# Optimization experiments

Hardware: AMD Instinct MI355X
Metric: run time of the kernel (lower is better)

The kernel has to match this reference:

```python
import jax, jax.numpy as jnp
import numpy as np

CAPACITY_FACTOR = 1.25
TOP_K = 2


def setup_inputs() -> dict:
    key = jax.random.key(0)
    ks = jax.random.split(key, 4)
    B, T, D, H, N = 8, 8192, 512, 512, 32
    x = jax.random.normal(ks[0], (B, T, D), jnp.float32)
    Wg = jax.random.normal(ks[1], (D, N), jnp.float32) * 0.02   # gate (no bias)
    W1 = jax.random.normal(ks[2], (N, D, H), jnp.float32) * 0.02  # stacked expert fc1
    b1 = jnp.zeros((N, H), jnp.float32)
    W2 = jax.random.normal(ks[3], (N, H, D), jnp.float32) * 0.02  # stacked expert fc2
    b2 = jnp.zeros((N, D), jnp.float32)
    return {"x": x, "Wg": Wg, "W1": W1, "b1": b1, "W2": W2, "b2": b2}


def _moe(x, Wg, W1, b1, W2, b2):
    B, T, D = x.shape
    N = Wg.shape[1]
    K = TOP_K
    BT = B * T
    BTK = BT * K
    C = int(np.ceil(CAPACITY_FACTOR * BTK / N))  # capacity per expert (static)

    x_flat = x.reshape(BT, D)
    probs = jax.nn.softmax(x_flat @ Wg, axis=-1)            # [BT, N]
    vals, idx = jax.lax.top_k(probs, K)                     # [BT, K]
    vals = vals / jnp.clip(vals.sum(-1, keepdims=True), 1e-9)  # normalize_gates

    # Assignments in the exact order of the original double loop: pos-major, j-minor.
    a = idx.reshape(BTK)                                    # expert id per assignment
    oh = jax.nn.one_hot(a, N, dtype=jnp.int32)              # [BTK, N]
    rank = jnp.cumsum(oh, axis=0) - oh                      # prior count for each expert
    pos = jnp.take_along_axis(rank, a[:, None], axis=1)[:, 0]  # slot within expert
    keep = pos < C                                          # capacity-limited dispatch
    dest = jnp.where(keep, a * C + pos, N * C)              # OOB sentinel -> dropped
    token = jnp.arange(BTK) // K                            # source token per assignment

    # Dispatch: scatter kept tokens into per-expert capacity buffers [N, C, D].
    buf = jnp.zeros((N * C, D), x.dtype).at[dest].set(x_flat[token], mode="drop")
    buf = buf.reshape(N, C, D)

    # Expert FFN (grouped GEMMs). FeedForwardExpert assumed Linear-ReLU-Linear.
    h = jax.nn.relu(jnp.einsum("ncd,ndh->nch", buf, W1) + b1[:, None, :])
    o = (jnp.einsum("nch,nhd->ncd", h, W2) + b2[:, None, :]).reshape(N * C, D)

    # Combine: gather expert outputs, weight by gates, scatter-add back by token.
    gathered = o[jnp.minimum(dest, N * C - 1)]              # dropped rows zeroed via w
    w = vals.reshape(BTK) * keep.astype(x.dtype)
    y_flat = jax.ops.segment_sum(gathered * w[:, None], token, num_segments=BT)
    contrib = jax.ops.segment_sum(w, token, num_segments=BT)
    # Tokens with no surviving assignment pass through unchanged.
    y_flat = jnp.where(contrib[:, None] <= 1e-12, x_flat, y_flat)
    return y_flat.reshape(B, T, D)


def reference(x, Wg, W1, b1, W2, b2):
    return _moe(x, Wg, W1, b1, W2, b2)
```

## Files before the change

### kernel.cpp

```cpp
#include <hip/hip_runtime.h>
#include <hip/hip_bf16.h>

#define BT 65536
#define DD 512
#define HH 512
#define NE 32
#define CAP 5120
#define BM 64
#define NRB 80

typedef float  f32x4  __attribute__((ext_vector_type(4)));
typedef short  bf16x8 __attribute__((ext_vector_type(8)));

__device__ __forceinline__ unsigned short f2bf(float f){
    unsigned int u = __builtin_bit_cast(unsigned int, f);
    unsigned int r = (u + 0x7fffu + ((u >> 16) & 1u)) >> 16;
    return (unsigned short)r;
}
__device__ __forceinline__ float bf2f(unsigned short h){
    unsigned int u = ((unsigned int)h) << 16;
    return __builtin_bit_cast(float, u);
}

__global__ __launch_bounds__(256) void k_wgprep(
    const float* __restrict__ Wg,
    unsigned short* __restrict__ WgHf, unsigned short* __restrict__ WgLf)
{
    int t = threadIdx.x;
    #pragma unroll
    for (int i = 0; i < 8; i++){
        int entry = i*256 + t;
        int ln = entry & 63;
        unsigned short h[8], l[8];
        #pragma unroll
        for (int j = 0; j < 8; j++){
            int d = ((entry >> 6) & 15)*32 + (ln >> 4)*8 + j;
            int e = (entry >> 10)*16 + (ln & 15);
            float v = Wg[d*NE + e];
            unsigned short hi = f2bf(v);
            h[j] = hi;
            l[j] = f2bf(v - bf2f(hi));
        }
        *(bf16x8*)(WgHf + (size_t)entry*8) = *(bf16x8*)h;
        *(bf16x8*)(WgLf + (size_t)entry*8) = *(bf16x8*)l;
    }
}

__global__ __launch_bounds__(256) void k_prep(
    const float* __restrict__ x, const float* __restrict__ Wg,
    const float* __restrict__ W1, const float* __restrict__ W2,
    const unsigned short* __restrict__ WgHf, const unsigned short* __restrict__ WgLf,
    unsigned short* __restrict__ W1f, unsigned short* __restrict__ W2f,
    int* __restrict__ counts, int* __restrict__ gsl, float* __restrict__ wts,
    unsigned char* __restrict__ flags, unsigned short* __restrict__ xb16)
{
    __shared__ unsigned char XH[32 * 1024];
    __shared__ unsigned char XL[32 * 1024];
    __shared__ float lg2[32 * 33];
    __shared__ int lcnt[NE], lbase[NE];

    int tid = threadIdx.x;

    if (blockIdx.x >= 2048){
        int b = blockIdx.x - 2048;
        int w = b >> 8;
        int e = (b >> 3) & 31;
        int kq = b & 7;
        const float* src = (w ? W2 : W1) + ((size_t)e << 18);
        unsigned short* dst = (w ? W2f : W1f) + ((size_t)e << 18);
        int n4 = (tid & 127) * 4;
        int kh = tid >> 7;
        #pragma unroll 1
        for (int kg = 0; kg < 4; kg++){
            int k0 = kq*64 + (kg*2 + kh)*8;
            float4 rows[8];
            #pragma unroll
            for (int j = 0; j < 8; j++)
                rows[j] = *(const float4*)&src[(size_t)(k0 + j)*512 + n4];
            unsigned short v0[8], v1[8], v2[8], v3[8];
            #pragma unroll
            for (int j = 0; j < 8; j++){
                v0[j] = f2bf(rows[j].x); v1[j] = f2bf(rows[j].y);
                v2[j] = f2bf(rows[j].z); v3[j] = f2bf(rows[j].w);
            }
            int kc = k0 >> 5, lb = ((k0 >> 3) & 3)*16;
            #pragma unroll
            for (int m = 0; m < 4; m++){
                int n = n4 + m;
                int nt = n >> 4, ln = lb + (n & 15);
                const unsigned short* vv = (m==0)?v0:(m==1)?v1:(m==2)?v2:v3;
                *(bf16x8*)(dst + (((size_t)(nt*16 + kc)*64 + ln) << 3)) = *(const bf16x8*)vv;
            }
        }
        return;
    }

    int t0 = blockIdx.x * 32;

    {
        int row = tid >> 3, seg = tid & 7;
        int tok = t0 + row;
        const float* sx = x + (size_t)tok*DD + seg*64;
        char* rbH = (char*)XH + row*1024;
        char* rbL = (char*)XL + row*1024;
        int rsw = (row & 7) << 4;
        #pragma unroll
        for (int jj = 0; jj < 8; jj++){
            float4 a = *(const float4*)(sx + jj*8);
            float4 b = *(const float4*)(sx + jj*8 + 4);
            unsigned short h[8], l[8];
            h[0]=f2bf(a.x); h[1]=f2bf(a.y); h[2]=f2bf(a.z); h[3]=f2bf(a.w);
            h[4]=f2bf(b.x); h[5]=f2bf(b.y); h[6]=f2bf(b.z); h[7]=f2bf(b.w);
            l[0]=f2bf(a.x-bf2f(h[0])); l[1]=f2bf(a.y-bf2f(h[1]));
            l[2]=f2bf(a.z-bf2f(h[2])); l[3]=f2bf(a.w-bf2f(h[3]));
            l[4]=f2bf(b.x-bf2f(h[4])); l[5]=f2bf(b.y-bf2f(h[5]));
            l[6]=f2bf(b.z-bf2f(h[6])); l[7]=f2bf(b.w-bf2f(h[7]));
            int chunk = seg*8 + jj;
            *(bf16x8*)(rbH + ((chunk << 4) ^ rsw)) = *(bf16x8*)h;
            *(bf16x8*)(rbL + ((chunk << 4) ^ rsw)) = *(bf16x8*)l;
            *(bf16x8*)(xb16 + (size_t)tok*DD + seg*64 + jj*8) = *(bf16x8*)h;
        }
    }
    if (tid < NE) lcnt[tid] = 0;
    __syncthreads();

    {
        int lane = tid & 63;
        int wv   = tid >> 6;
        int lg   = lane >> 4, ll = lane & 15;
        int ef = wv >> 1, tf = wv & 1;
        const unsigned short* Ah = WgHf + ef*8192;
        const unsigned short* Al = WgLf + ef*8192;
        int tokl = tf*16 + ll;
        f32x4 acc = (f32x4)0.f;
        #pragma unroll 1
        for (int kc = 0; kc < 16; kc++){
            bf16x8 ah = *(const bf16x8*)(Ah + kc*512 + lane*8);
            bf16x8 al = *(const bf16x8*)(Al + kc*512 + lane*8);
            int bofs = (64*kc + 16*lg) ^ ((tokl & 7) << 4);
            bf16x8 bh = *(const bf16x8*)((char*)XH + tokl*1024 + bofs);
            bf16x8 bl = *(const bf16x8*)((char*)XL + tokl*1024 + bofs);
            acc = __builtin_amdgcn_mfma_f32_16x16x32_bf16(ah, bh, acc, 0, 0, 0);
            acc = __builtin_amdgcn_mfma_f32_16x16x32_bf16(ah, bl, acc, 0, 0, 0);
            acc = __builtin_amdgcn_mfma_f32_16x16x32_bf16(al, bh, acc, 0, 0, 0);
        }
        #pragma unroll
        for (int i = 0; i < 4; i++)
            lg2[tokl*33 + ef*16 + lg*4 + i] = acc[i];
    }
    __syncthreads();

    float w1 = 0.f, w2 = 0.f;
    int i1 = 0, i2 = 0, s1 = 0, s2 = 0;
    bool act = (tid < 32);
    if (act){
        int tok = t0 + tid;
        float acc[NE];
        #pragma unroll
        for (int n = 0; n < NE; n++) acc[n] = lg2[tid*33 + n];

        float v1 = -1e30f; i1 = -1;
        #pragma unroll
        for (int n = 0; n < NE; n++) if (acc[n] > v1){ v1 = acc[n]; i1 = n; }
        float v2 = -1e30f; i2 = -1;
        #pragma unroll
        for (int n = 0; n < NE; n++) if (n != i1 && acc[n] > v2){ v2 = acc[n]; i2 = n; }
        float v3 = -1e30f;
        #pragma unroll
        for (int n = 0; n < NE; n++) if (n != i1 && n != i2 && acc[n] > v3) v3 = acc[n];

        if (v2 - v3 >= 1e-4f){
            double ex  = exp((double)v2 - (double)v1);
            double inv = 1.0 / (1.0 + ex);
            w1 = (float)inv; w2 = (float)(ex * inv);
        } else {
            const float* xr = x + (size_t)tok * DD;
            float thresh = v2 - 1e-3f;
            unsigned cmask = 0u;
            #pragma unroll
            for (int n = 0; n < NE; n++) cmask |= (acc[n] >= thresh) ? (1u << n) : 0u;
            double dv1 = -1.0e300, dv2 = -1.0e300; int di1 = -1, di2 = -1;
            #pragma unroll 1
            for (int n = 0; n < NE; n++){
                if (!((cmask >> n) & 1u)) continue;
                double q0 = 0.0, q1 = 0.0, q2 = 0.0, q3 = 0.0;
                #pragma unroll 4
                for (int d = 0; d < DD; d += 4){
                    q0 = fma((double)xr[d+0], (double)Wg[(size_t)(d+0)*NE + n], q0);
                    q1 = fma((double)xr[d+1], (double)Wg[(size_t)(d+1)*NE + n], q1);
                    q2 = fma((double)xr[d+2], (double)Wg[(size_t)(d+2)*NE + n], q2);
                    q3 = fma((double)xr[d+3], (double)Wg[(size_t)(d+3)*NE + n], q3);
                }
                double sv = (q0 + q1) + (q2 + q3);
                if (sv > dv1){ dv2 = dv1; di2 = di1; dv1 = sv; di1 = n; }
                else if (sv > dv2){ dv2 = sv; di2 = n; }
            }
            i1 = di1; i2 = di2;
            double ex  = exp(dv2 - dv1);
            double inv = 1.0 / (1.0 + ex);
            w1 = (float)inv; w2 = (float)(ex * inv);
        }
        s1 = atomicAdd(&lcnt[i1], 1);
        s2 = atomicAdd(&lcnt[i2], 1);
    }
    __syncthreads();
    if (tid < NE && lcnt[tid] > 0) lbase[tid] = atomicAdd(&counts[tid], lcnt[tid]);
    __syncthreads();
    if (act){
        int tok = t0 + tid;
        int g1 = lbase[i1] + s1;
        int g2 = lbase[i2] + s2;
        bool k1 = g1 < CAP, k2 = g2 < CAP;
        if (k1){ gsl[i1*CAP + g1] = tok;               wts[i1*CAP + g1] = w1; }
        if (k2){ gsl[i2*CAP + g2] = tok | (1 << 20);   wts[i2*CAP + g2] = w2; }
        flags[tok] = (unsigned char)((k1 ? 1 : 0) | (k2 ? 2 : 0));
    }
}

__global__ __launch_bounds__(512, 4) void k_ffn(
    const unsigned short* __restrict__ xb16,
    const unsigned short* __restrict__ W1f,
    const unsigned short* __restrict__ W2f,
    const float* __restrict__ b1, const float* __restrict__ b2,
    const int* __restrict__ counts,
    const int* __restrict__ gsl, const float* __restrict__ wts,
    float* __restrict__ y, unsigned short* __restrict__ y2h)
{
    __shared__ unsigned char AH[64 * 1024];

    int p  = blockIdx.x;
    int s  = p >> 3;
    int e  = ((s / NRB) << 3) | (p & 7);
    int rb = s % NRB;

    int cnt = counts[e]; if (cnt > CAP) cnt = CAP;
    int r0 = rb * BM;
    if (r0 >= cnt) return;

    int tid  = threadIdx.x;
    int lane = tid & 63;
    int wv   = tid >> 6;
    int lg   = lane >> 4;
    int ll   = lane & 15;

    {
        int row = tid >> 3, seg = tid & 7;
        int gr  = r0 + row;
        char* rowb = (char*)AH + row * 1024;
        int rsw = (row & 7) << 4;
        if (gr < cnt){
            int tk = gsl[e*CAP + gr] & 0xFFFFF;
            const uint4* src = (const uint4*)(xb16 + (size_t)tk*DD + seg*64);
            #pragma unroll
            for (int j = 0; j < 8; j++){
                uint4 v = src[j];
                int chunk = seg*8 + j;
                *(uint4*)(rowb + ((chunk << 4) ^ rsw)) = v;
            }
        } else {
            uint4 zz; zz.x = zz.y = zz.z = zz.w = 0u;
            #pragma unroll
            for (int j = 0; j < 8; j++){
                int chunk = seg*8 + j;
                *(uint4*)(rowb + ((chunk << 4) ^ rsw)) = zz;
            }
        }
    }
    __syncthreads();

    f32x4 acc[4][4];
    #pragma unroll
    for (int a2 = 0; a2 < 4; a2++)
        #pragma unroll
        for (int tt = 0; tt < 4; tt++)
            acc[a2][tt] = (f32x4)0.f;

    {
        const unsigned short* Wa = W1f + ((size_t)e << 18) + (size_t)wv*32768;
        bf16x8 f0[4], f1[4];
        #pragma unroll
        for (int a2 = 0; a2 < 4; a2++)
            f0[a2] = *(const bf16x8*)(Wa + a2*8192 + lane*8);
        #pragma unroll 1
        for (int c = 0; c < 16; c += 2){
            #pragma unroll
            for (int a2 = 0; a2 < 4; a2++)
                f1[a2] = *(const bf16x8*)(Wa + a2*8192 + (c+1)*512 + lane*8);
            {
                bf16x8 bx[4];
                #pragma unroll
                for (int tt = 0; tt < 4; tt++){
                    int tok = tt*16 + ll;
                    int bofs = (64*c + 16*lg) ^ ((tok & 7) << 4);
                    bx[tt] = *(const bf16x8*)((char*)AH + tok*1024 + bofs);
                }
                __builtin_amdgcn_s_setprio(1);
                #pragma unroll
                for (int a2 = 0; a2 < 4; a2++)
                    #pragma unroll
                    for (int tt = 0; tt < 4; tt++)
                        acc[a2][tt] = __builtin_amdgcn_mfma_f32_16x16x32_bf16(f0[a2], bx[tt], acc[a2][tt], 0, 0, 0);
                __builtin_amdgcn_s_setprio(0);
            }
            if (c + 2 < 16){
                #pragma unroll
                for (int a2 = 0; a2 < 4; a2++)
                    f0[a2] = *(const bf16x8*)(Wa + a2*8192 + (c+2)*512 + lane*8);
            }
            {
                bf16x8 bx[4];
                #pragma unroll
                for (int tt = 0; tt < 4; tt++){
                    int tok = tt*16 + ll;
                    int bofs = (64*(c+1) + 16*lg) ^ ((tok & 7) << 4);
                    bx[tt] = *(const bf16x8*)((char*)AH + tok*1024 + bofs);
                }
                __builtin_amdgcn_s_setprio(1);
                #pragma unroll
                for (int a2 = 0; a2 < 4; a2++)
                    #pragma unroll
                    for (int tt = 0; tt < 4; tt++)
                        acc[a2][tt] = __builtin_amdgcn_mfma_f32_16x16x32_bf16(f1[a2], bx[tt], acc[a2][tt], 0, 0, 0);
                __builtin_amdgcn_s_setprio(0);
            }
        }
    }
    __syncthreads();

    #pragma unroll
    for (int a2 = 0; a2 < 4; a2++){
        int n0 = wv*64 + a2*16 + lg*4;
        float4 bv = *(const float4*)(b1 + e*HH + n0);
        #pragma unroll
        for (int tt = 0; tt < 4; tt++){
            int tok = tt*16 + ll;
            float h0 = acc[a2][tt][0] + bv.x; h0 = h0 > 0.f ? h0 : 0.f;
            float h1 = acc[a2][tt][1] + bv.y; h1 = h1 > 0.f ? h1 : 0.f;
            float h2 = acc[a2][tt][2] + bv.z; h2 = h2 > 0.f ? h2 : 0.f;
            float h3 = acc[a2][tt][3] + bv.w; h3 = h3 > 0.f ? h3 : 0.f;
            uint2 pk;
            pk.x = (unsigned)f2bf(h0) | ((unsigned)f2bf(h1) << 16);
            pk.y = (unsigned)f2bf(h2) | ((unsigned)f2bf(h3) << 16);
            int bofs = (n0*2) ^ ((tok & 7) << 4);
            *(uint2*)((char*)AH + tok*1024 + bofs) = pk;
            acc[a2][tt] = (f32x4)0.f;
        }
    }
    __syncthreads();

    {
        const unsigned short* Wb = W2f + ((size_t)e << 18) + (size_t)wv*32768;
        bf16x8 f0[4], f1[4];
        #pragma unroll
        for (int b_ = 0; b_ < 4; b_++)
            f0[b_] = *(const bf16x8*)(Wb + b_*8192 + lane*8);
        #pragma unroll 1
        for (int kc = 0; kc < 16; kc += 2){
            #pragma unroll
            for (int b_ = 0; b_ < 4; b_++)
                f1[b_] = *(const bf16x8*)(Wb + b_*8192 + (kc+1)*512 + lane*8);
            {
                bf16x8 ah[4];
                #pragma unroll
                for (int tt = 0; tt < 4; tt++){
                    int tok = tt*16 + ll;
                    int bofs = (64*kc + 16*lg) ^ ((tok & 7) << 4);
                    ah[tt] = *(const bf16x8*)((char*)AH + tok*1024 + bofs);
                }
                __builtin_amdgcn_s_setprio(1);
                #pragma unroll
                for (int b_ = 0; b_ < 4; b_++)
                    #pragma unroll
                    for (int tt = 0; tt < 4; tt++)
                        acc[b_][tt] = __builtin_amdgcn_mfma_f32_16x16x32_bf16(ah[tt], f0[b_], acc[b_][tt], 0, 0, 0);
                __builtin_amdgcn_s_setprio(0);
            }
            if (kc + 2 < 16){
                #pragma unroll
                for (int b_ = 0; b_ < 4; b_++)
                    f0[b_] = *(const bf16x8*)(Wb + b_*8192 + (kc+2)*512 + lane*8);
            }
            {
                bf16x8 ah[4];
                #pragma unroll
                for (int tt = 0; tt < 4; tt++){
                    int tok = tt*16 + ll;
                    int bofs = (64*(kc+1) + 16*lg) ^ ((tok & 7) << 4);
                    ah[tt] = *(const bf16x8*)((char*)AH + tok*1024 + bofs);
                }
                __builtin_amdgcn_s_setprio(1);
                #pragma unroll
                for (int b_ = 0; b_ < 4; b_++)
                    #pragma unroll
                    for (int tt = 0; tt < 4; tt++)
                        acc[b_][tt] = __builtin_amdgcn_mfma_f32_16x16x32_bf16(ah[tt], f1[b_], acc[b_][tt], 0, 0, 0);
                __builtin_amdgcn_s_setprio(0);
            }
        }
    }

    float bb[4];
    #pragma unroll
    for (int b_ = 0; b_ < 4; b_++)
        bb[b_] = b2[e*DD + wv*64 + b_*16 + ll];

    #pragma unroll
    for (int tt = 0; tt < 4; tt++){
        #pragma unroll
        for (int i = 0; i < 4; i++){
            int rl = tt*16 + lg*4 + i;
            int gr = r0 + rl;
            if (gr < cnt){
                int   v  = gsl[e*CAP + gr];
                int   tk = v & 0xFFFFF;
                float w  = wts[e*CAP + gr];
                if (v >> 20){
                    unsigned short* dst = y2h + (size_t)tk * DD;
                    #pragma unroll
                    for (int b_ = 0; b_ < 4; b_++){
                        int col = wv*64 + b_*16 + ll;
                        dst[col] = f2bf(w * (acc[b_][tt][i] + bb[b_]));
                    }
                } else {
                    float* dst = y + (size_t)tk * DD;
                    #pragma unroll
                    for (int b_ = 0; b_ < 4; b_++){
                        int col = wv*64 + b_*16 + ll;
                        dst[col] = w * (acc[b_][tt][i] + bb[b_]);
                    }
                }
            }
        }
    }
}

__global__ __launch_bounds__(256) void k_comb(
    const float* __restrict__ x, const unsigned short* __restrict__ y2h,
    const unsigned char* __restrict__ flags, float* __restrict__ y)
{
    const float4* x4  = (const float4*)x;
    const uint2*  y24 = (const uint2*)y2h;
    float4* y4 = (float4*)y;
    int nthreads = gridDim.x * 256;
    int g = blockIdx.x * 256 + threadIdx.x;
    #pragma unroll 1
    for (long long idx = g; idx < (long long)BT * 128; idx += nthreads){
        int t = (int)(idx >> 7);
        int f = flags[t];
        if (f == 3){
            float4 a = y4[idx];
            uint2 p = y24[idx];
            a.x += bf2f((unsigned short)(p.x & 0xFFFF));
            a.y += bf2f((unsigned short)(p.x >> 16));
            a.z += bf2f((unsigned short)(p.y & 0xFFFF));
            a.w += bf2f((unsigned short)(p.y >> 16));
            y4[idx] = a;
        } else if (f == 2){
            uint2 p = y24[idx];
            float4 a;
            a.x = bf2f((unsigned short)(p.x & 0xFFFF));
            a.y = bf2f((unsigned short)(p.x >> 16));
            a.z = bf2f((unsigned short)(p.y & 0xFFFF));
            a.w = bf2f((unsigned short)(p.y >> 16));
            y4[idx] = a;
        } else if (f == 0){
            y4[idx] = x4[idx];
        }
    }
}

extern "C" void kernel_launch(void* const* d_in, const int* in_sizes, int n_in,
                              void* d_out, int out_size, void* d_ws, size_t ws_size,
                              hipStream_t stream)
{
    const float* x  = (const float*)d_in[0];
    const float* Wg = (const float*)d_in[1];
    const float* W1 = (const float*)d_in[2];
    const float* b1 = (const float*)d_in[3];
    const float* W2 = (const float*)d_in[4];
    const float* b2 = (const float*)d_in[5];
    float* y = (float*)d_out;

    char* ws = (char*)d_ws;
    unsigned short* W1f = (unsigned short*)(ws);
    unsigned short* W2f = (unsigned short*)(ws + 16777216);
    size_t b3 = 33554432;
    int*   counts = (int*)  (ws + b3);
    int*   gsl    = (int*)  (ws + b3 + 256);
    float* wts    = (float*)(ws + b3 + 256 + 655360);
    unsigned char* flags = (unsigned char*)(ws + b3 + 256 + 2*655360);
    unsigned short* WgHf = (unsigned short*)(ws + b3 + 256 + 2*655360 + 65536);
    unsigned short* WgLf = (unsigned short*)(ws + b3 + 256 + 2*655360 + 65536 + 32768);
    unsigned short* xb16 = (unsigned short*)(ws + 35651584);
    unsigned short* y2h  = (unsigned short*)(ws + 35651584 + 67108864);

    hipMemsetAsync(counts, 0, 256, stream);
    hipLaunchKernelGGL(k_wgprep, dim3(1), dim3(256), 0, stream, Wg, WgHf, WgLf);
    hipLaunchKernelGGL(k_prep, dim3(2048 + 512), dim3(256), 0, stream,
                       x, Wg, W1, W2, WgHf, WgLf, W1f, W2f, counts, gsl, wts, flags, xb16);
    hipLaunchKernelGGL(k_ffn,  dim3(NE*NRB), dim3(512), 0, stream,
                       xb16, W1f, W2f, b1, b2, counts, gsl, wts, y, y2h);
    hipLaunchKernelGGL(k_comb, dim3(2048), dim3(256), 0, stream, x, y2h, flags, y);
}
```

Baseline: 394.7 us.

## Compute gate logits directly from registers, drop LDS staging, 64 tokens per block

The gating kernel no longer stages the hi/lo bf16 split of x in 64 KB of shared memory. Each wave now converts its own 16 tokens' rows in registers and feeds them straight into the MFMA gate GEMM, covering both expert halves per wave. Each block handles 64 tokens instead of 32, which halves the gating blocks, and the Wg prep kernel is spread over 8 blocks instead of looping in one. This removes the LDS round-trip, a barrier and the heavy LDS footprint that limited occupancy. In exchange, each wave reloads the Wg fragments from global memory or cache, and the x reads are more strided per lane.

```diff
diff --git a/kernel.cpp b/kernel.cpp
--- a/kernel.cpp
+++ b/kernel.cpp
@@ -26,24 +26,20 @@
     const float* __restrict__ Wg,
     unsigned short* __restrict__ WgHf, unsigned short* __restrict__ WgLf)
 {
-    int t = threadIdx.x;
+    int entry = blockIdx.x * 256 + threadIdx.x;
+    int ln = entry & 63;
+    unsigned short h[8], l[8];
     #pragma unroll
-    for (int i = 0; i < 8; i++){
-        int entry = i*256 + t;
-        int ln = entry & 63;
-        unsigned short h[8], l[8];
-        #pragma unroll
-        for (int j = 0; j < 8; j++){
-            int d = ((entry >> 6) & 15)*32 + (ln >> 4)*8 + j;
-            int e = (entry >> 10)*16 + (ln & 15);
-            float v = Wg[d*NE + e];
-            unsigned short hi = f2bf(v);
-            h[j] = hi;
-            l[j] = f2bf(v - bf2f(hi));
-        }
-        *(bf16x8*)(WgHf + (size_t)entry*8) = *(bf16x8*)h;
-        *(bf16x8*)(WgLf + (size_t)entry*8) = *(bf16x8*)l;
-    }
+    for (int j = 0; j < 8; j++){
+        int d = ((entry >> 6) & 15)*32 + (ln >> 4)*8 + j;
+        int e = (entry >> 10)*16 + (ln & 15);
+        float v = Wg[d*NE + e];
+        unsigned short hi = f2bf(v);
+        h[j] = hi;
+        l[j] = f2bf(v - bf2f(hi));
+    }
+    *(bf16x8*)(WgHf + (size_t)entry*8) = *(bf16x8*)h;
+    *(bf16x8*)(WgLf + (size_t)entry*8) = *(bf16x8*)l;
 }
 
 __global__ __launch_bounds__(256) void k_prep(
@@ -54,15 +50,13 @@
     int* __restrict__ counts, int* __restrict__ gsl, float* __restrict__ wts,
     unsigned char* __restrict__ flags, unsigned short* __restrict__ xb16)
 {
-    __shared__ unsigned char XH[32 * 1024];
-    __shared__ unsigned char XL[32 * 1024];
-    __shared__ float lg2[32 * 33];
+    __shared__ float lg2[64 * 33];
     __shared__ int lcnt[NE], lbase[NE];
 
     int tid = threadIdx.x;
 
-    if (blockIdx.x >= 2048){
-        int b = blockIdx.x - 2048;
+    if (blockIdx.x >= 1024){
+        int b = blockIdx.x - 1024;
         int w = b >> 8;
         int e = (b >> 3) & 31;
         int kq = b & 7;
@@ -95,19 +89,20 @@
         return;
     }
 
-    int t0 = blockIdx.x * 32;
-
+    int t0 = blockIdx.x * 64;
     {
-        int row = tid >> 3, seg = tid & 7;
-        int tok = t0 + row;
-        const float* sx = x + (size_t)tok*DD + seg*64;
-        char* rbH = (char*)XH + row*1024;
-        char* rbL = (char*)XL + row*1024;
-        int rsw = (row & 7) << 4;
-        #pragma unroll
-        for (int jj = 0; jj < 8; jj++){
-            float4 a = *(const float4*)(sx + jj*8);
-            float4 b = *(const float4*)(sx + jj*8 + 4);
+        int lane = tid & 63;
+        int wv   = tid >> 6;
+        int lg   = lane >> 4, ll = lane & 15;
+        int tokl = wv*16 + ll;
+        const float* xr = x + (size_t)(t0 + tokl)*DD;
+
+        f32x4 acc0 = (f32x4)0.f, acc1 = (f32x4)0.f;
+        #pragma unroll 4
+        for (int kc = 0; kc < 16; kc++){
+            int d0 = kc*32 + lg*8;
+            float4 a = *(const float4*)(xr + d0);
+            float4 b = *(const float4*)(xr + d0 + 4);
             unsigned short h[8], l[8];
             h[0]=f2bf(a.x); h[1]=f2bf(a.y); h[2]=f2bf(a.z); h[3]=f2bf(a.w);
             h[4]=f2bf(b.x); h[5]=f2bf(b.y); h[6]=f2bf(b.z); h[7]=f2bf(b.w);
@@ -115,44 +110,31 @@
             l[2]=f2bf(a.z-bf2f(h[2])); l[3]=f2bf(a.w-bf2f(h[3]));
             l[4]=f2bf(b.x-bf2f(h[4])); l[5]=f2bf(b.y-bf2f(h[5]));
             l[6]=f2bf(b.z-bf2f(h[6])); l[7]=f2bf(b.w-bf2f(h[7]));
-            int chunk = seg*8 + jj;
-            *(bf16x8*)(rbH + ((chunk << 4) ^ rsw)) = *(bf16x8*)h;
-            *(bf16x8*)(rbL + ((chunk << 4) ^ rsw)) = *(bf16x8*)l;
-            *(bf16x8*)(xb16 + (size_t)tok*DD + seg*64 + jj*8) = *(bf16x8*)h;
+            bf16x8 bh = *(bf16x8*)h, bl = *(bf16x8*)l;
+            *(bf16x8*)(xb16 + (size_t)(t0 + tokl)*DD + d0) = bh;
+            bf16x8 ah0 = *(const bf16x8*)(WgHf + ((size_t)(kc*64 + lane) << 3));
+            bf16x8 al0 = *(const bf16x8*)(WgLf + ((size_t)(kc*64 + lane) << 3));
+            bf16x8 ah1 = *(const bf16x8*)(WgHf + ((size_t)(1024 + kc*64 + lane) << 3));
+            bf16x8 al1 = *(const bf16x8*)(WgLf + ((size_t)(1024 + kc*64 + lane) << 3));
+            acc0 = __builtin_amdgcn_mfma_f32_16x16x32_bf16(ah0, bh, acc0, 0, 0, 0);
+            acc0 = __builtin_amdgcn_mfma_f32_16x16x32_bf16(ah0, bl, acc0, 0, 0, 0);
+            acc0 = __builtin_amdgcn_mfma_f32_16x16x32_bf16(al0, bh, acc0, 0, 0, 0);
+            acc1 = __builtin_amdgcn_mfma_f32_16x16x32_bf16(ah1, bh, acc1, 0, 0, 0);
+            acc1 = __builtin_amdgcn_mfma_f32_16x16x32_bf16(ah1, bl, acc1, 0, 0, 0);
+            acc1 = __builtin_amdgcn_mfma_f32_16x16x32_bf16(al1, bh, acc1, 0, 0, 0);
+        }
+        #pragma unroll
+        for (int i = 0; i < 4; i++){
+            lg2[tokl*33 +      lg*4 + i] = acc0[i];
+            lg2[tokl*33 + 16 + lg*4 + i] = acc1[i];
         }
     }
     if (tid < NE) lcnt[tid] = 0;
-    __syncthreads();
-
-    {
-        int lane = tid & 63;
-        int wv   = tid >> 6;
-        int lg   = lane >> 4, ll = lane & 15;
-        int ef = wv >> 1, tf = wv & 1;
-        const unsigned short* Ah = WgHf + ef*8192;
-        const unsigned short* Al = WgLf + ef*8192;
-        int tokl = tf*16 + ll;
-        f32x4 acc = (f32x4)0.f;
-        #pragma unroll 1
-        for (int kc = 0; kc < 16; kc++){
-            bf16x8 ah = *(const bf16x8*)(Ah + kc*512 + lane*8);
-            bf16x8 al = *(const bf16x8*)(Al + kc*512 + lane*8);
-            int bofs = (64*kc + 16*lg) ^ ((tokl & 7) << 4);
-            bf16x8 bh = *(const bf16x8*)((char*)XH + tokl*1024 + bofs);
-            bf16x8 bl = *(const bf16x8*)((char*)XL + tokl*1024 + bofs);
-            acc = __builtin_amdgcn_mfma_f32_16x16x32_bf16(ah, bh, acc, 0, 0, 0);
-            acc = __builtin_amdgcn_mfma_f32_16x16x32_bf16(ah, bl, acc, 0, 0, 0);
-            acc = __builtin_amdgcn_mfma_f32_16x16x32_bf16(al, bh, acc, 0, 0, 0);
-        }
-        #pragma unroll
-        for (int i = 0; i < 4; i++)
-            lg2[tokl*33 + ef*16 + lg*4 + i] = acc[i];
-    }
     __syncthreads();
 
     float w1 = 0.f, w2 = 0.f;
     int i1 = 0, i2 = 0, s1 = 0, s2 = 0;
-    bool act = (tid < 32);
+    bool act = (tid < 64);
     if (act){
         int tok = t0 + tid;
         float acc[NE];
@@ -495,8 +477,8 @@
     unsigned short* y2h  = (unsigned short*)(ws + 35651584 + 67108864);
 
     hipMemsetAsync(counts, 0, 256, stream);
-    hipLaunchKernelGGL(k_wgprep, dim3(1), dim3(256), 0, stream, Wg, WgHf, WgLf);
-    hipLaunchKernelGGL(k_prep, dim3(2048 + 512), dim3(256), 0, stream,
+    hipLaunchKernelGGL(k_wgprep, dim3(8), dim3(256), 0, stream, Wg, WgHf, WgLf);
+    hipLaunchKernelGGL(k_prep, dim3(1024 + 512), dim3(256), 0, stream,
                        x, Wg, W1, W2, WgHf, WgLf, W1f, W2f, counts, gsl, wts, flags, xb16);
     hipLaunchKernelGGL(k_ffn,  dim3(NE*NRB), dim3(512), 0, stream,
                        xb16, W1f, W2f, b1, b2, counts, gsl, wts, y, y2h);
```

Result: faster. 356.1 us (-9.8%).
